# Kernel optimization log

Measured on AMD Instinct MI355X. Metric: run time of the kernel, lower is better.

Reference implementation:

```python
import jax, jax.numpy as jnp
import numpy as np
from jax import lax

B, S, C = 128, 512, 16
V, CV = 50000, 100
E, CE = 100, 30
H = 128        # hidden per direction (hidden_dim=256 // 2)
T = 17         # tagset size
NF = 25        # filters per char-conv
LSTM_IN = E + 3 * NF  # 175


def setup_inputs() -> dict:
    key = jax.random.key(0)
    ks = jax.random.split(key, 25)
    sc = 0.1
    inp = {
        "x": jax.random.randint(ks[0], (B, S), 0, V),
        "char_x": jax.random.randint(ks[1], (B, S, C), 0, CV),
        "tags": jax.random.randint(ks[2], (B, S), 0, T),
        "mask": jnp.ones((B, S), dtype=bool),
        "word_emb": jax.random.normal(ks[3], (V, E), jnp.float32) * sc,
        "char_emb": jax.random.normal(ks[4], (CV, CE), jnp.float32) * sc,
        "conv2_W": jax.random.normal(ks[5], (NF, CE, 2), jnp.float32) * sc,
        "conv2_b": jnp.zeros((NF,), jnp.float32),
        "conv3_W": jax.random.normal(ks[6], (NF, CE, 3), jnp.float32) * sc,
        "conv3_b": jnp.zeros((NF,), jnp.float32),
        "conv4_W": jax.random.normal(ks[7], (NF, CE, 4), jnp.float32) * sc,
        "conv4_b": jnp.zeros((NF,), jnp.float32),
        "W_ih_f": jax.random.normal(ks[8], (4 * H, LSTM_IN), jnp.float32) * sc,
        "W_hh_f": jax.random.normal(ks[9], (4 * H, H), jnp.float32) * sc,
        "b_f": jnp.zeros((4 * H,), jnp.float32),
        "W_ih_b": jax.random.normal(ks[10], (4 * H, LSTM_IN), jnp.float32) * sc,
        "W_hh_b": jax.random.normal(ks[11], (4 * H, H), jnp.float32) * sc,
        "b_b": jnp.zeros((4 * H,), jnp.float32),
        "h2t_W": jax.random.normal(ks[12], (T, 2 * H), jnp.float32) * sc,
        "h2t_b": jnp.zeros((T,), jnp.float32),
        "crf_start": jax.random.normal(ks[13], (T,), jnp.float32) * sc,
        "crf_end": jax.random.normal(ks[14], (T,), jnp.float32) * sc,
        "crf_trans": jax.random.normal(ks[15], (T, T), jnp.float32) * sc,
    }
    return inp


def _char_conv(ce, W, b):
    # ce: [BS, CE, C], W: [O, I, K] -> [BS, O] after relu + max-over-time
    out = lax.conv_general_dilated(ce, W, (1,), 'VALID',
                                   dimension_numbers=('NCH', 'OIH', 'NCH'))
    out = jax.nn.relu(out + b[None, :, None])
    return jnp.max(out, axis=-1)


def _lstm_dir(xs, W_ih, W_hh, b, reverse):
    # xs: [B, S, D] -> hs [B, S, H]; PyTorch gate order i,f,g,o
    xs_t = jnp.swapaxes(xs, 0, 1)  # [S, B, D]
    if reverse:
        xs_t = xs_t[::-1]
    pre = jnp.einsum('sbd,gd->sbg', xs_t, W_ih) + b  # hoist input projection
    h0 = jnp.zeros((xs.shape[0], H), xs.dtype)

    def step(carry, p_t):
        h, c = carry
        g = p_t + h @ W_hh.T
        i = jax.nn.sigmoid(g[:, :H])
        f = jax.nn.sigmoid(g[:, H:2 * H])
        gg = jnp.tanh(g[:, 2 * H:3 * H])
        o = jax.nn.sigmoid(g[:, 3 * H:])
        c = f * c + i * gg
        h = o * jnp.tanh(c)
        return (h, c), h

    _, hs = lax.scan(step, (h0, h0), pre)
    if reverse:
        hs = hs[::-1]
    return jnp.swapaxes(hs, 0, 1)


def _crf_nll(emissions, tags, mask, start, end, trans):
    # emissions [B,S,T]; returns sum over batch of -log p(tags | emissions)
    maskf = mask.astype(emissions.dtype)
    # ---- numerator (gold score) ----
    em_sc = jnp.take_along_axis(emissions, tags[..., None], axis=2)[..., 0]  # [B,S]
    tr_sc = trans[tags[:, :-1], tags[:, 1:]]                                  # [B,S-1]
    last_idx = jnp.sum(mask, axis=1).astype(jnp.int32) - 1
    last_tag = tags[jnp.arange(tags.shape[0]), last_idx]
    score = (start[tags[:, 0]] + em_sc[:, 0]
             + jnp.sum(maskf[:, 1:] * (tr_sc + em_sc[:, 1:]), axis=1)
             + end[last_tag])
    # ---- partition via forward-algorithm scan ----
    em_t = jnp.swapaxes(emissions, 0, 1)  # [S,B,T]
    alpha0 = start[None, :] + em_t[0]     # [B,T]

    def step(alpha, inputs):
        e_t, m_t = inputs  # [B,T], [B]
        new = jax.nn.logsumexp(alpha[:, :, None] + trans[None] + e_t[:, None, :], axis=1)
        alpha = jnp.where(m_t[:, None], new, alpha)
        return alpha, None

    alpha, _ = lax.scan(step, alpha0, (em_t[1:], jnp.swapaxes(mask, 0, 1)[1:]))
    logZ = jax.nn.logsumexp(alpha + end[None, :], axis=1)
    return jnp.sum(logZ - score)


def reference(x, char_x, tags, mask, word_emb, char_emb,
              conv2_W, conv2_b, conv3_W, conv3_b, conv4_W, conv4_b,
              W_ih_f, W_hh_f, b_f, W_ih_b, W_hh_b, b_b,
              h2t_W, h2t_b, crf_start, crf_end, crf_trans):
    # word + char features
    we = word_emb[x]                                     # [B,S,E]
    ce = char_emb[char_x].reshape(B * S, C, CE)          # [BS,C,CE]
    ce = jnp.swapaxes(ce, 1, 2)                          # [BS,CE,C]
    cf = jnp.concatenate([_char_conv(ce, conv2_W, conv2_b),
                          _char_conv(ce, conv3_W, conv3_b),
                          _char_conv(ce, conv4_W, conv4_b)], axis=1)
    cf = cf.reshape(B, S, 3 * NF)
    feats = jnp.concatenate([we, cf], axis=2)            # [B,S,175]
    # BiLSTM
    h_fwd = _lstm_dir(feats, W_ih_f, W_hh_f, b_f, reverse=False)
    h_bwd = _lstm_dir(feats, W_ih_b, W_hh_b, b_b, reverse=True)
    h = jnp.concatenate([h_fwd, h_bwd], axis=2)          # [B,S,2H]
    emissions = jnp.einsum('bsh,th->bst', h, h2t_W) + h2t_b
    # CRF NLL (model returns -crf(...), torchcrf reduction='sum')
    return _crf_nll(emissions, tags, mask, crf_start, crf_end, crf_trans)
```

## Files before the change

kernel.cpp:

```cpp
#include <hip/hip_runtime.h>
#include <hip/hip_bf16.h>

#define B_ 128
#define S_ 512
#define C_ 16
#define E_ 100
#define CE_ 30
#define NF_ 25
#define H_ 128
#define T_ 17
#define LSTM_IN_ 175
#define KP_ 192
#define G4_ 512

typedef __hip_bfloat16 bf16;
typedef short bf16x8 __attribute__((ext_vector_type(8)));
typedef float f32x4 __attribute__((ext_vector_type(4)));

__device__ __forceinline__ float bf2f(unsigned short u){
  union { unsigned int i; float f; } v; v.i = ((unsigned int)u) << 16; return v.f;
}
__device__ __forceinline__ float sigm_f(float x){
  float e = __expf(-x);
  return __builtin_amdgcn_rcpf(1.0f + e);
}
__device__ __forceinline__ float tanh_f(float x){
  x = fminf(15.0f, fmaxf(-15.0f, x));
  float e = __expf(-2.0f*x);
  return (1.0f - e) * __builtin_amdgcn_rcpf(1.0f + e);
}
__device__ __forceinline__ short bf16bits(float f){
  bf16 b = __float2bfloat16(f);
  return *(short*)&b;
}

__global__ __launch_bounds__(256) void zero_pad_kernel(bf16* __restrict__ feats){
  int task = blockIdx.x*256 + threadIdx.x;
  int word = task / 17;
  int col = LSTM_IN_ + (task - word*17);
  feats[(size_t)word*KP_ + col] = __float2bfloat16(0.0f);
}

__global__ __launch_bounds__(256) void word_emb_kernel(const int* __restrict__ x,
    const float* __restrict__ wemb, bf16* __restrict__ feats){
  int word = blockIdx.x*2 + (threadIdx.x>>7);
  int e = threadIdx.x & 127;
  if (e < E_) feats[(size_t)word*KP_ + e] = __float2bfloat16(wemb[(size_t)x[word]*E_ + e]);
}

template<int KW>
__global__ __launch_bounds__(256) void char_conv_kernel(const int* __restrict__ char_x,
    const float* __restrict__ cemb, const float* __restrict__ W,
    const float* __restrict__ bias, bf16* __restrict__ feats, int out_off){
  int task = blockIdx.x*256 + threadIdx.x;
  int word = task / NF_;
  int fi = task - word*NF_;
  const int* cx = char_x + word*C_;
  float w[KW*CE_];
  #pragma unroll
  for (int i=0;i<KW*CE_;++i) w[i] = W[fi*CE_*KW + i];
  const int NP = C_ - KW + 1;
  float acc[C_ - KW + 1];
  #pragma unroll
  for (int p=0;p<NP;++p) acc[p] = 0.0f;
  #pragma unroll
  for (int c=0;c<C_;++c){
    int ci = cx[c];
    const float* ce = cemb + ci*CE_;
    #pragma unroll
    for (int e=0;e<CE_;++e){
      float v = ce[e];
      #pragma unroll
      for (int dx=0;dx<KW;++dx){
        int p = c - dx;
        if (p >= 0 && p < NP) acc[p] = fmaf(v, w[e*KW+dx], acc[p]);
      }
    }
  }
  float m = acc[0];
  #pragma unroll
  for (int p=1;p<NP;++p) m = fmaxf(m, acc[p]);
  feats[(size_t)word*KP_ + out_off + fi] = __float2bfloat16(fmaxf(0.0f, m + bias[fi]));
}

__global__ __launch_bounds__(192) void wpack_kernel(const float* __restrict__ Wf,
    const float* __restrict__ Wb, bf16* __restrict__ wpk){
  int g = blockIdx.x;
  int k = threadIdx.x;
  float v = 0.0f;
  if (k < LSTM_IN_) v = (g < 512) ? Wf[g*LSTM_IN_ + k] : Wb[(g-512)*LSTM_IN_ + k];
  wpk[(size_t)g*KP_ + k] = __float2bfloat16(v);
}

__global__ __launch_bounds__(256) void whh_pack_kernel(const float* __restrict__ Wf,
    const float* __restrict__ Wb, bf16* __restrict__ wpk2){
  int idx = blockIdx.x*256 + threadIdx.x;
  int dir = idx >> 16;
  int rem = idx & 65535;
  const float* W = dir ? Wb : Wf;
  wpk2[idx] = __float2bfloat16(W[rem]);
}

__global__ __launch_bounds__(256, 3) void pre_gemm_mfma(const bf16* __restrict__ feats,
    const bf16* __restrict__ wpk, const float* __restrict__ bf_,
    const float* __restrict__ bb_, bf16* __restrict__ pre){
  __shared__ __align__(16) short lds[16384];
  int br = blockIdx.x;
  int bc = blockIdx.y;
  int dir = bc >> 2;
  int g0 = (bc & 3) * 128;
  const float* bias = dir ? bb_ : bf_;
  int tid = threadIdx.x;
  int wave = tid >> 6, lane = tid & 63;
  int wr = wave >> 1, wc = wave & 1;
  int lrow = lane & 15, lkb = lane >> 4;
  const bf16* Arow = feats + (size_t)br*128*KP_;
  const bf16* Brow = wpk + (size_t)(dir*512 + g0)*KP_;

  auto stage = [&](int bufbase, int k0){
    int s0 = wave*2, s1 = s0 + 1;
    __builtin_amdgcn_global_load_lds(
        (const __attribute__((address_space(1))) void*)(Arow + (size_t)(s0*16 + lrow)*KP_ + k0 + lkb*8),
        (__attribute__((address_space(3))) void*)&lds[bufbase + s0*512], 16, 0, 0);
    __builtin_amdgcn_global_load_lds(
        (const __attribute__((address_space(1))) void*)(Arow + (size_t)(s1*16 + lrow)*KP_ + k0 + lkb*8),
        (__attribute__((address_space(3))) void*)&lds[bufbase + s1*512], 16, 0, 0);
    __builtin_amdgcn_global_load_lds(
        (const __attribute__((address_space(1))) void*)(Brow + (size_t)(s0*16 + lrow)*KP_ + k0 + lkb*8),
        (__attribute__((address_space(3))) void*)&lds[bufbase + 4096 + s0*512], 16, 0, 0);
    __builtin_amdgcn_global_load_lds(
        (const __attribute__((address_space(1))) void*)(Brow + (size_t)(s1*16 + lrow)*KP_ + k0 + lkb*8),
        (__attribute__((address_space(3))) void*)&lds[bufbase + 4096 + s1*512], 16, 0, 0);
  };

  f32x4 acc[4][4];
  #pragma unroll
  for (int i=0;i<4;++i)
    #pragma unroll
    for (int j=0;j<4;++j) acc[i][j] = (f32x4){0.f,0.f,0.f,0.f};

  stage(0, 0);
  __syncthreads();
  int cur = 0;
  for (int t = 0; t < 6; ++t){
    if (t < 5) stage((cur^1)*8192, (t+1)*32);
    const short* A  = &lds[cur*8192];
    const short* Bv = &lds[cur*8192 + 4096];
    bf16x8 af[4], bfr[4];
    #pragma unroll
    for (int i=0;i<4;++i) af[i]  = *(const bf16x8*)&A[(wr*4+i)*512 + lane*8];
    #pragma unroll
    for (int j=0;j<4;++j) bfr[j] = *(const bf16x8*)&Bv[(wc*4+j)*512 + lane*8];
    #pragma unroll
    for (int i=0;i<4;++i)
      #pragma unroll
      for (int j=0;j<4;++j)
        acc[i][j] = __builtin_amdgcn_mfma_f32_16x16x32_bf16(af[i], bfr[j], acc[i][j], 0, 0, 0);
    __syncthreads();
    cur ^= 1;
  }

  int col_l = lane & 15;
  int row_l = (lane >> 4) * 4;
  float bias_v[4];
  #pragma unroll
  for (int j=0;j<4;++j) bias_v[j] = bias[g0 + wc*64 + j*16 + col_l];
  #pragma unroll
  for (int i=0;i<4;++i){
    #pragma unroll
    for (int q=0;q<4;++q){
      int r = wr*64 + i*16 + row_l + q;
      #pragma unroll
      for (int j=0;j<4;++j){
        int cbyte = (wc*64 + j*16 + col_l) * 2;
        int addr = r*256 + (cbyte ^ ((r & 7) << 4));
        *(short*)((char*)lds + addr) = bf16bits(acc[i][j][q] + bias_v[j]);
      }
    }
  }
  __syncthreads();
  int r = tid >> 1, half = tid & 1;
  int word = br*128 + r;
  int bidx = word >> 9, sidx = word & 511;
  bf16* dst = pre + ((size_t)(dir*B_ + bidx)*S_ + sidx)*G4_ + g0 + half*64;
  #pragma unroll
  for (int k=0;k<8;++k){
    int boff = (half*128 + k*16) ^ ((r & 7) << 4);
    int4 v = *(const int4*)((const char*)lds + r*256 + boff);
    *(int4*)((char*)dst + k*16) = v;
  }
}

__global__ __launch_bounds__(512) void lstm_mfma_kernel(
    const bf16* __restrict__ pre, const bf16* __restrict__ wpk2,
    bf16* __restrict__ hs){
  int blk = blockIdx.x;
  int dir = blk & 1;
  int bg  = blk >> 1;
  int tid = threadIdx.x;
  int w = tid >> 6, l = tid & 63;
  int lm = l & 15, lk = l >> 4;
  int gcol = 16*w + lm;

  bf16x8 Bf[4][4];
  {
    const bf16* Wd = wpk2 + (size_t)dir*512*128;
    #pragma unroll
    for (int ct=0; ct<4; ++ct)
      #pragma unroll
      for (int kk=0; kk<4; ++kk)
        Bf[ct][kk] = *(const bf16x8*)(Wd + (ct*128 + gcol)*128 + 32*kk + lk*8);
  }

  __shared__ __align__(16) short h_sh[2][2048];
  for (int i = tid; i < 1024; i += 512) ((int*)h_sh[0])[i] = 0;

  float c[4] = {0.f, 0.f, 0.f, 0.f};
  const bf16* preB = pre + (size_t)(dir*B_ + bg*16) * (S_*G4_);
  bf16* hsB = hs + (size_t)(dir*B_ + bg*16) * (S_*H_);

  unsigned short pfA[16], pfB[16];
  auto LOADPF = [&](unsigned short (&pf)[16], int idx){
    #pragma unroll
    for (int q=0;q<4;++q){
      #pragma unroll
      for (int ct=0;ct<4;++ct)
        pf[q*4+ct] = *(const unsigned short*)(preB
            + ((size_t)((lk*4+q)*S_ + idx))*G4_ + ct*128 + gcol);
    }
  };

  auto STEP = [&](unsigned short (&pfuse)[16], int s, const short* src, short* dst){
    int idx = dir ? (S_-1-s) : s;
    f32x4 a0, a1, a2, a3;
    #pragma unroll
    for (int q=0;q<4;++q){
      a0[q] = bf2f(pfuse[q*4+0]);
      a1[q] = bf2f(pfuse[q*4+1]);
      a2[q] = bf2f(pfuse[q*4+2]);
      a3[q] = bf2f(pfuse[q*4+3]);
    }
    int sp = (s+2 < S_) ? s+2 : s;
    int idxp = dir ? (S_-1-sp) : sp;
    LOADPF(pfuse, idxp);
    #pragma unroll
    for (int kk=0;kk<4;++kk){
      int sc = ((4*kk + lk) ^ lm) & 15;
      bf16x8 af = *(const bf16x8*)((const char*)src + lm*256 + sc*16);
      a0 = __builtin_amdgcn_mfma_f32_16x16x32_bf16(af, Bf[0][kk], a0, 0, 0, 0);
      a1 = __builtin_amdgcn_mfma_f32_16x16x32_bf16(af, Bf[1][kk], a1, 0, 0, 0);
      a2 = __builtin_amdgcn_mfma_f32_16x16x32_bf16(af, Bf[2][kk], a2, 0, 0, 0);
      a3 = __builtin_amdgcn_mfma_f32_16x16x32_bf16(af, Bf[3][kk], a3, 0, 0, 0);
    }
    float hv[4];
    #pragma unroll
    for (int q=0;q<4;++q){
      float iv = sigm_f(a0[q]);
      float fv = sigm_f(a1[q]);
      float gv = tanh_f(a2[q]);
      float ov = sigm_f(a3[q]);
      c[q] = fmaf(fv, c[q], iv*gv);
      hv[q] = ov * tanh_f(c[q]);
    }
    #pragma unroll
    for (int q=0;q<4;++q){
      int b = lk*4 + q;
      int scw = ((gcol >> 3) ^ b) & 15;
      *(short*)((char*)dst + b*256 + scw*16 + (gcol & 7)*2) = bf16bits(hv[q]);
      hsB[((size_t)b*S_ + idx)*H_ + gcol] = __float2bfloat16(hv[q]);
    }
    asm volatile("s_waitcnt lgkmcnt(0)" ::: "memory");
    __builtin_amdgcn_s_barrier();
    asm volatile("" ::: "memory");
  };

  __syncthreads();
  LOADPF(pfA, dir ? (S_-1) : 0);
  LOADPF(pfB, dir ? (S_-2) : 1);
  for (int s = 0; s < S_; s += 2){
    STEP(pfA, s,   h_sh[0], h_sh[1]);
    STEP(pfB, s+1, h_sh[1], h_sh[0]);
  }
}

__global__ __launch_bounds__(256) void emis_kernel(const bf16* __restrict__ hs,
    const float* __restrict__ W, const float* __restrict__ bias, float* __restrict__ em){
  int task = blockIdx.x*256 + threadIdx.x;
  int word = task / T_;
  int t = task - word*T_;
  const ushort4* hf = (const ushort4*)(hs + (size_t)word*H_);
  const ushort4* hb = (const ushort4*)(hs + (size_t)(B_*S_ + word)*H_);
  const float* w0 = W + t*2*H_;
  float acc = bias[t];
  #pragma unroll
  for (int j4=0;j4<32;++j4){
    ushort4 u = hf[j4];
    float4 w4 = *(const float4*)&w0[j4*4];
    acc = fmaf(bf2f(u.x),w4.x,acc); acc = fmaf(bf2f(u.y),w4.y,acc);
    acc = fmaf(bf2f(u.z),w4.z,acc); acc = fmaf(bf2f(u.w),w4.w,acc);
  }
  #pragma unroll
  for (int j4=0;j4<32;++j4){
    ushort4 u = hb[j4];
    float4 w4 = *(const float4*)&w0[H_ + j4*4];
    acc = fmaf(bf2f(u.x),w4.x,acc); acc = fmaf(bf2f(u.y),w4.y,acc);
    acc = fmaf(bf2f(u.z),w4.z,acc); acc = fmaf(bf2f(u.w),w4.w,acc);
  }
  em[(size_t)word*T_ + t] = acc;
}

__global__ __launch_bounds__(256) void score_kernel(const int* __restrict__ tags,
    const float* __restrict__ em, const float* __restrict__ start,
    const float* __restrict__ end_, const float* __restrict__ trans,
    float* __restrict__ score){
  int b = blockIdx.x;
  int tid = threadIdx.x;
  const int* tg = tags + b*S_;
  const float* eb = em + (size_t)b*S_*T_;
  float s = 0.0f;
  for (int t = tid; t < S_; t += 256){
    int cur = tg[t];
    s += eb[(size_t)t*T_ + cur];
    if (t > 0) s += trans[tg[t-1]*T_ + cur];
  }
  if (tid == 0) s += start[tg[0]] + end_[tg[S_-1]];
  __shared__ float red[256];
  red[tid] = s; __syncthreads();
  for (int off=128; off; off>>=1){
    if (tid < off) red[tid] += red[tid+off];
    __syncthreads();
  }
  if (tid == 0) score[b] = red[0];
}

__global__ __launch_bounds__(64) void crf_alpha_kernel(const float* __restrict__ em,
    const float* __restrict__ start, const float* __restrict__ end_,
    const float* __restrict__ trans, float* __restrict__ logZ){
  int b = blockIdx.x;
  int j = threadIdx.x;
  __shared__ float al[T_];
  const float* eb = em + (size_t)b*S_*T_;
  float tcol[T_];
  if (j < T_){
    #pragma unroll
    for (int i=0;i<T_;++i) tcol[i] = trans[i*T_ + j];
    al[j] = start[j] + eb[j];
  }
  float e_cur = (j < T_) ? eb[T_ + j] : 0.0f;
  for (int s=1;s<S_;++s){
    float e_nxt = (j < T_ && s+1 < S_) ? eb[(size_t)(s+1)*T_ + j] : 0.0f;
    if (j < T_){
      float av[T_];
      float m = -1e30f;
      #pragma unroll
      for (int i=0;i<T_;++i){ av[i] = al[i] + tcol[i]; m = fmaxf(m, av[i]); }
      float sum = 0.0f;
      #pragma unroll
      for (int i=0;i<T_;++i) sum += __expf(av[i]-m);
      float nv = m + __logf(sum) + e_cur;
      al[j] = nv;
    }
    e_cur = e_nxt;
  }
  if (j == 0){
    float m = -1e30f;
    float v[T_];
    #pragma unroll
    for (int i=0;i<T_;++i){ v[i] = al[i] + end_[i]; m = fmaxf(m, v[i]); }
    float sum = 0.0f;
    #pragma unroll
    for (int i=0;i<T_;++i) sum += __expf(v[i]-m);
    logZ[b] = m + __logf(sum);
  }
}

__global__ __launch_bounds__(128) void final_kernel(const float* __restrict__ logZ,
    const float* __restrict__ score, float* __restrict__ out){
  int tid = threadIdx.x;
  float v = logZ[tid] - score[tid];
  __shared__ float red[128];
  red[tid] = v; __syncthreads();
  for (int off=64; off; off>>=1){
    if (tid < off) red[tid] += red[tid+off];
    __syncthreads();
  }
  if (tid == 0) out[0] = red[0];
}

extern "C" void kernel_launch(void* const* d_in, const int* in_sizes, int n_in,
                              void* d_out, int out_size, void* d_ws, size_t ws_size,
                              hipStream_t stream) {
  const int*   x       = (const int*)  d_in[0];
  const int*   char_x  = (const int*)  d_in[1];
  const int*   tags    = (const int*)  d_in[2];
  const float* wemb    = (const float*)d_in[4];
  const float* cemb    = (const float*)d_in[5];
  const float* c2W     = (const float*)d_in[6];
  const float* c2b     = (const float*)d_in[7];
  const float* c3W     = (const float*)d_in[8];
  const float* c3b     = (const float*)d_in[9];
  const float* c4W     = (const float*)d_in[10];
  const float* c4b     = (const float*)d_in[11];
  const float* Wih_f   = (const float*)d_in[12];
  const float* Whh_f   = (const float*)d_in[13];
  const float* b_f     = (const float*)d_in[14];
  const float* Wih_b   = (const float*)d_in[15];
  const float* Whh_b   = (const float*)d_in[16];
  const float* b_b     = (const float*)d_in[17];
  const float* h2tW    = (const float*)d_in[18];
  const float* h2tb    = (const float*)d_in[19];
  const float* crf_s   = (const float*)d_in[20];
  const float* crf_e   = (const float*)d_in[21];
  const float* crf_t   = (const float*)d_in[22];
  float* out = (float*)d_out;

  const size_t NEEDED = 168035328ULL;
  if (ws_size < NEEDED) return;
  char* wsb = (char*)d_ws;
  bf16*  pre   = (bf16*)(wsb);
  bf16*  feats = (bf16*)(wsb + 134217728);
  bf16*  wpk   = (bf16*)(wsb + 159383552);
  bf16*  hs    = (bf16*)(wsb + 134217728);
  float* em    = (float*)(wsb);
  float* score = (float*)(wsb + 167772160);
  float* logZ  = (float*)(wsb + 167772672);
  bf16*  wpk2  = (bf16*)(wsb + 167773184);

  zero_pad_kernel<<<4352, 256, 0, stream>>>(feats);
  word_emb_kernel<<<32768, 256, 0, stream>>>(x, wemb, feats);
  char_conv_kernel<2><<<6400, 256, 0, stream>>>(char_x, cemb, c2W, c2b, feats, E_);
  char_conv_kernel<3><<<6400, 256, 0, stream>>>(char_x, cemb, c3W, c3b, feats, E_ + NF_);
  char_conv_kernel<4><<<6400, 256, 0, stream>>>(char_x, cemb, c4W, c4b, feats, E_ + 2*NF_);
  wpack_kernel<<<1024, 192, 0, stream>>>(Wih_f, Wih_b, wpk);
  whh_pack_kernel<<<512, 256, 0, stream>>>(Whh_f, Whh_b, wpk2);
  pre_gemm_mfma<<<dim3(512, 8), 256, 0, stream>>>(feats, wpk, b_f, b_b, pre);
  lstm_mfma_kernel<<<16, 512, 0, stream>>>(pre, wpk2, hs);
  emis_kernel<<<4352, 256, 0, stream>>>(hs, h2tW, h2tb, em);
  score_kernel<<<128, 256, 0, stream>>>(tags, em, crf_s, crf_e, crf_t, score);
  crf_alpha_kernel<<<128, 64, 0, stream>>>(em, crf_s, crf_e, crf_t, logZ);
  final_kernel<<<1, 128, 0, stream>>>(logZ, score, out);
}
```

Before: 1.597 ms.

## Fuse emission projection into LSTM recurrence and pair CRF batches per block

Each LSTM step now computes its direction's share of the hidden-to-tag projection with extra MFMAs on the h tile already held in LDS. Forward and backward partial emissions go to separate buffers and are summed in the score and CRF kernels. This removes the hs write-back and the separate emission kernel. It also strength-reduces the prefetch addressing, packs two batches per CRF block with tree reductions, and adds a few MFMAs to the serial critical path of the recurrence.

```diff
diff --git a/kernel.cpp b/kernel.cpp
--- a/kernel.cpp
+++ b/kernel.cpp
@@ -99,6 +99,16 @@
   int rem = idx & 65535;
   const float* W = dir ? Wb : Wf;
   wpk2[idx] = __float2bfloat16(W[rem]);
+}
+
+__global__ __launch_bounds__(256) void wem_pack_kernel(const float* __restrict__ h2tW,
+    bf16* __restrict__ wem){
+  int idx = blockIdx.x*256 + threadIdx.x;
+  int d = idx >> 12;
+  int rem = idx & 4095;
+  int t = rem >> 7, k = rem & 127;
+  float v = (t < T_) ? h2tW[t*(2*H_) + d*H_ + k] : 0.0f;
+  wem[idx] = __float2bfloat16(v);
 }
 
 __global__ __launch_bounds__(256, 3) void pre_gemm_mfma(const bf16* __restrict__ feats,
@@ -193,7 +203,8 @@
 
 __global__ __launch_bounds__(512) void lstm_mfma_kernel(
     const bf16* __restrict__ pre, const bf16* __restrict__ wpk2,
-    bf16* __restrict__ hs){
+    const bf16* __restrict__ wem, const float* __restrict__ h2tb,
+    float* __restrict__ em_f, float* __restrict__ em_b){
   int blk = blockIdx.x;
   int dir = blk & 1;
   int bg  = blk >> 1;
@@ -208,30 +219,61 @@
     #pragma unroll
     for (int ct=0; ct<4; ++ct)
       #pragma unroll
-      for (int kk=0; kk<4; ++kk)
+      for (int kk=0; kk<4; ++kk){
         Bf[ct][kk] = *(const bf16x8*)(Wd + (ct*128 + gcol)*128 + 32*kk + lk*8);
-  }
+        asm volatile("" : "+v"(Bf[ct][kk]));
+      }
+  }
+  int tag = w*16 + lm;
+  bf16x8 Ef[4];
+  {
+    int trow = (w < 2) ? tag : 0;
+    #pragma unroll
+    for (int kk=0; kk<4; ++kk){
+      Ef[kk] = *(const bf16x8*)(wem + ((size_t)dir*32 + trow)*128 + 32*kk + lk*8);
+      asm volatile("" : "+v"(Ef[kk]));
+    }
+  }
+  float embias = 0.0f;
+  if (dir == 0 && w < 2 && tag < T_) embias = h2tb[tag];
 
   __shared__ __align__(16) short h_sh[2][2048];
   for (int i = tid; i < 1024; i += 512) ((int*)h_sh[0])[i] = 0;
 
   float c[4] = {0.f, 0.f, 0.f, 0.f};
   const bf16* preB = pre + (size_t)(dir*B_ + bg*16) * (S_*G4_);
-  bf16* hsB = hs + (size_t)(dir*B_ + bg*16) * (S_*H_);
+  int sd  = dir ? -1 : 1;
+  int sdG = sd * G4_;
+  int sdT = sd * T_;
+  int idx0 = dir ? (S_-1) : 0;
+
+  const bf16 *p0 = preB + ((size_t)(lk*4+0)*S_ + idx0)*G4_ + gcol;
+  const bf16 *p1 = preB + ((size_t)(lk*4+1)*S_ + idx0)*G4_ + gcol;
+  const bf16 *p2 = preB + ((size_t)(lk*4+2)*S_ + idx0)*G4_ + gcol;
+  const bf16 *p3 = preB + ((size_t)(lk*4+3)*S_ + idx0)*G4_ + gcol;
+
+  float* emBase = (dir ? em_b : em_f) + (size_t)(bg*16)*S_*T_;
+  float *e0 = emBase + ((size_t)(lk*4+0)*S_ + idx0)*T_ + tag;
+  float *e1 = emBase + ((size_t)(lk*4+1)*S_ + idx0)*T_ + tag;
+  float *e2 = emBase + ((size_t)(lk*4+2)*S_ + idx0)*T_ + tag;
+  float *e3 = emBase + ((size_t)(lk*4+3)*S_ + idx0)*T_ + tag;
 
   unsigned short pfA[16], pfB[16];
-  auto LOADPF = [&](unsigned short (&pf)[16], int idx){
-    #pragma unroll
-    for (int q=0;q<4;++q){
-      #pragma unroll
-      for (int ct=0;ct<4;++ct)
-        pf[q*4+ct] = *(const unsigned short*)(preB
-            + ((size_t)((lk*4+q)*S_ + idx))*G4_ + ct*128 + gcol);
-    }
+  auto LOADPF = [&](unsigned short (&pf)[16], bool g){
+    if (g){
+      pf[0]  = *(const unsigned short*)(p0);     pf[1]  = *(const unsigned short*)(p0+128);
+      pf[2]  = *(const unsigned short*)(p0+256); pf[3]  = *(const unsigned short*)(p0+384);
+      pf[4]  = *(const unsigned short*)(p1);     pf[5]  = *(const unsigned short*)(p1+128);
+      pf[6]  = *(const unsigned short*)(p1+256); pf[7]  = *(const unsigned short*)(p1+384);
+      pf[8]  = *(const unsigned short*)(p2);     pf[9]  = *(const unsigned short*)(p2+128);
+      pf[10] = *(const unsigned short*)(p2+256); pf[11] = *(const unsigned short*)(p2+384);
+      pf[12] = *(const unsigned short*)(p3);     pf[13] = *(const unsigned short*)(p3+128);
+      pf[14] = *(const unsigned short*)(p3+256); pf[15] = *(const unsigned short*)(p3+384);
+    }
+    p0 += sdG; p1 += sdG; p2 += sdG; p3 += sdG;
   };
 
   auto STEP = [&](unsigned short (&pfuse)[16], int s, const short* src, short* dst){
-    int idx = dir ? (S_-1-s) : s;
     f32x4 a0, a1, a2, a3;
     #pragma unroll
     for (int q=0;q<4;++q){
@@ -240,18 +282,26 @@
       a2[q] = bf2f(pfuse[q*4+2]);
       a3[q] = bf2f(pfuse[q*4+3]);
     }
-    int sp = (s+2 < S_) ? s+2 : s;
-    int idxp = dir ? (S_-1-sp) : sp;
-    LOADPF(pfuse, idxp);
+    LOADPF(pfuse, s+2 < S_);
+    bf16x8 af[4];
     #pragma unroll
     for (int kk=0;kk<4;++kk){
       int sc = ((4*kk + lk) ^ lm) & 15;
-      bf16x8 af = *(const bf16x8*)((const char*)src + lm*256 + sc*16);
-      a0 = __builtin_amdgcn_mfma_f32_16x16x32_bf16(af, Bf[0][kk], a0, 0, 0, 0);
-      a1 = __builtin_amdgcn_mfma_f32_16x16x32_bf16(af, Bf[1][kk], a1, 0, 0, 0);
-      a2 = __builtin_amdgcn_mfma_f32_16x16x32_bf16(af, Bf[2][kk], a2, 0, 0, 0);
-      a3 = __builtin_amdgcn_mfma_f32_16x16x32_bf16(af, Bf[3][kk], a3, 0, 0, 0);
-    }
+      af[kk] = *(const bf16x8*)((const char*)src + lm*256 + sc*16);
+      a0 = __builtin_amdgcn_mfma_f32_16x16x32_bf16(af[kk], Bf[0][kk], a0, 0, 0, 0);
+      a1 = __builtin_amdgcn_mfma_f32_16x16x32_bf16(af[kk], Bf[1][kk], a1, 0, 0, 0);
+      a2 = __builtin_amdgcn_mfma_f32_16x16x32_bf16(af[kk], Bf[2][kk], a2, 0, 0, 0);
+      a3 = __builtin_amdgcn_mfma_f32_16x16x32_bf16(af[kk], Bf[3][kk], a3, 0, 0, 0);
+    }
+    if (w < 2 && s > 0){
+      f32x4 emq;
+      emq[0]=embias; emq[1]=embias; emq[2]=embias; emq[3]=embias;
+      #pragma unroll
+      for (int kk=0;kk<4;++kk)
+        emq = __builtin_amdgcn_mfma_f32_16x16x32_bf16(af[kk], Ef[kk], emq, 0, 0, 0);
+      if (tag < T_){ *e0 = emq[0]; *e1 = emq[1]; *e2 = emq[2]; *e3 = emq[3]; }
+    }
+    if (s > 0){ e0 += sdT; e1 += sdT; e2 += sdT; e3 += sdT; }
     float hv[4];
     #pragma unroll
     for (int q=0;q<4;++q){
@@ -267,7 +317,6 @@
       int b = lk*4 + q;
       int scw = ((gcol >> 3) ^ b) & 15;
       *(short*)((char*)dst + b*256 + scw*16 + (gcol & 7)*2) = bf16bits(hv[q]);
-      hsB[((size_t)b*S_ + idx)*H_ + gcol] = __float2bfloat16(hv[q]);
     }
     asm volatile("s_waitcnt lgkmcnt(0)" ::: "memory");
     __builtin_amdgcn_s_barrier();
@@ -275,52 +324,39 @@
   };
 
   __syncthreads();
-  LOADPF(pfA, dir ? (S_-1) : 0);
-  LOADPF(pfB, dir ? (S_-2) : 1);
+  LOADPF(pfA, true);
+  LOADPF(pfB, true);
   for (int s = 0; s < S_; s += 2){
     STEP(pfA, s,   h_sh[0], h_sh[1]);
     STEP(pfB, s+1, h_sh[1], h_sh[0]);
   }
-}
-
-__global__ __launch_bounds__(256) void emis_kernel(const bf16* __restrict__ hs,
-    const float* __restrict__ W, const float* __restrict__ bias, float* __restrict__ em){
-  int task = blockIdx.x*256 + threadIdx.x;
-  int word = task / T_;
-  int t = task - word*T_;
-  const ushort4* hf = (const ushort4*)(hs + (size_t)word*H_);
-  const ushort4* hb = (const ushort4*)(hs + (size_t)(B_*S_ + word)*H_);
-  const float* w0 = W + t*2*H_;
-  float acc = bias[t];
-  #pragma unroll
-  for (int j4=0;j4<32;++j4){
-    ushort4 u = hf[j4];
-    float4 w4 = *(const float4*)&w0[j4*4];
-    acc = fmaf(bf2f(u.x),w4.x,acc); acc = fmaf(bf2f(u.y),w4.y,acc);
-    acc = fmaf(bf2f(u.z),w4.z,acc); acc = fmaf(bf2f(u.w),w4.w,acc);
-  }
-  #pragma unroll
-  for (int j4=0;j4<32;++j4){
-    ushort4 u = hb[j4];
-    float4 w4 = *(const float4*)&w0[H_ + j4*4];
-    acc = fmaf(bf2f(u.x),w4.x,acc); acc = fmaf(bf2f(u.y),w4.y,acc);
-    acc = fmaf(bf2f(u.z),w4.z,acc); acc = fmaf(bf2f(u.w),w4.w,acc);
-  }
-  em[(size_t)word*T_ + t] = acc;
+  if (w < 2){
+    f32x4 emq;
+    emq[0]=embias; emq[1]=embias; emq[2]=embias; emq[3]=embias;
+    #pragma unroll
+    for (int kk=0;kk<4;++kk){
+      int sc = ((4*kk + lk) ^ lm) & 15;
+      bf16x8 af = *(const bf16x8*)((const char*)h_sh[0] + lm*256 + sc*16);
+      emq = __builtin_amdgcn_mfma_f32_16x16x32_bf16(af, Ef[kk], emq, 0, 0, 0);
+    }
+    if (tag < T_){ *e0 = emq[0]; *e1 = emq[1]; *e2 = emq[2]; *e3 = emq[3]; }
+  }
 }
 
 __global__ __launch_bounds__(256) void score_kernel(const int* __restrict__ tags,
-    const float* __restrict__ em, const float* __restrict__ start,
+    const float* __restrict__ em_f, const float* __restrict__ em_b,
+    const float* __restrict__ start,
     const float* __restrict__ end_, const float* __restrict__ trans,
     float* __restrict__ score){
   int b = blockIdx.x;
   int tid = threadIdx.x;
   const int* tg = tags + b*S_;
-  const float* eb = em + (size_t)b*S_*T_;
+  const float* ef = em_f + (size_t)b*S_*T_;
+  const float* eb = em_b + (size_t)b*S_*T_;
   float s = 0.0f;
   for (int t = tid; t < S_; t += 256){
     int cur = tg[t];
-    s += eb[(size_t)t*T_ + cur];
+    s += ef[(size_t)t*T_ + cur] + eb[(size_t)t*T_ + cur];
     if (t > 0) s += trans[tg[t-1]*T_ + cur];
   }
   if (tid == 0) s += start[tg[0]] + end_[tg[S_-1]];
@@ -333,40 +369,59 @@
   if (tid == 0) score[b] = red[0];
 }
 
-__global__ __launch_bounds__(64) void crf_alpha_kernel(const float* __restrict__ em,
+__global__ __launch_bounds__(64) void crf_alpha_kernel(const float* __restrict__ em_f,
+    const float* __restrict__ em_b,
     const float* __restrict__ start, const float* __restrict__ end_,
     const float* __restrict__ trans, float* __restrict__ logZ){
-  int b = blockIdx.x;
-  int j = threadIdx.x;
-  __shared__ float al[T_];
-  const float* eb = em + (size_t)b*S_*T_;
+  int pair = blockIdx.x;
+  int lane = threadIdx.x;
+  int half = lane >> 5;
+  int j = lane & 31;
+  int b = pair*2 + half;
+  bool act = j < T_;
+  const float* ef = em_f + (size_t)b*S_*T_;
+  const float* eb = em_b + (size_t)b*S_*T_;
+  __shared__ float al2[2][32];
   float tcol[T_];
-  if (j < T_){
+  if (act){
     #pragma unroll
     for (int i=0;i<T_;++i) tcol[i] = trans[i*T_ + j];
-    al[j] = start[j] + eb[j];
-  }
-  float e_cur = (j < T_) ? eb[T_ + j] : 0.0f;
+    al2[half][j] = start[j] + ef[j] + eb[j];
+  }
+  float ecur = act ? (ef[T_ + j] + eb[T_ + j]) : 0.0f;
+  float enxt = (act && 2 < S_) ? (ef[2*T_ + j] + eb[2*T_ + j]) : 0.0f;
   for (int s=1;s<S_;++s){
-    float e_nxt = (j < T_ && s+1 < S_) ? eb[(size_t)(s+1)*T_ + j] : 0.0f;
-    if (j < T_){
+    float enew = (act && s+2 < S_) ? (ef[(size_t)(s+2)*T_ + j] + eb[(size_t)(s+2)*T_ + j]) : 0.0f;
+    if (act){
       float av[T_];
-      float m = -1e30f;
-      #pragma unroll
-      for (int i=0;i<T_;++i){ av[i] = al[i] + tcol[i]; m = fmaxf(m, av[i]); }
-      float sum = 0.0f;
-      #pragma unroll
-      for (int i=0;i<T_;++i) sum += __expf(av[i]-m);
-      float nv = m + __logf(sum) + e_cur;
-      al[j] = nv;
-    }
-    e_cur = e_nxt;
+      #pragma unroll
+      for (int i=0;i<T_;++i) av[i] = al2[half][i] + tcol[i];
+      float m = fmaxf(
+        fmaxf(fmaxf(fmaxf(av[0],av[1]),fmaxf(av[2],av[3])),
+              fmaxf(fmaxf(av[4],av[5]),fmaxf(av[6],av[7]))),
+        fmaxf(fmaxf(fmaxf(av[8],av[9]),fmaxf(av[10],av[11])),
+              fmaxf(fmaxf(av[12],av[13]),fmaxf(fmaxf(av[14],av[15]),av[16]))));
+      float s0=0.f,s1=0.f,s2=0.f,s3=0.f;
+      #pragma unroll
+      for (int i=0;i<16;i+=4){
+        s0 += __expf(av[i]-m);   s1 += __expf(av[i+1]-m);
+        s2 += __expf(av[i+2]-m); s3 += __expf(av[i+3]-m);
+      }
+      s0 += __expf(av[16]-m);
+      float sum = (s0+s1)+(s2+s3);
+      al2[half][j] = m + __logf(sum) + ecur;
+    }
+    ecur = enxt; enxt = enew;
   }
   if (j == 0){
-    float m = -1e30f;
     float v[T_];
     #pragma unroll
-    for (int i=0;i<T_;++i){ v[i] = al[i] + end_[i]; m = fmaxf(m, v[i]); }
+    for (int i=0;i<T_;++i) v[i] = al2[half][i] + end_[i];
+    float m = fmaxf(
+      fmaxf(fmaxf(fmaxf(v[0],v[1]),fmaxf(v[2],v[3])),
+            fmaxf(fmaxf(v[4],v[5]),fmaxf(v[6],v[7]))),
+      fmaxf(fmaxf(fmaxf(v[8],v[9]),fmaxf(v[10],v[11])),
+            fmaxf(fmaxf(v[12],v[13]),fmaxf(fmaxf(v[14],v[15]),v[16]))));
     float sum = 0.0f;
     #pragma unroll
     for (int i=0;i<T_;++i) sum += __expf(v[i]-m);
@@ -414,17 +469,18 @@
   const float* crf_t   = (const float*)d_in[22];
   float* out = (float*)d_out;
 
-  const size_t NEEDED = 168035328ULL;
+  const size_t NEEDED = 160056320ULL;
   if (ws_size < NEEDED) return;
   char* wsb = (char*)d_ws;
   bf16*  pre   = (bf16*)(wsb);
   bf16*  feats = (bf16*)(wsb + 134217728);
+  float* em_f  = (float*)(wsb + 134217728);
+  float* em_b  = (float*)(wsb + 138674176);
   bf16*  wpk   = (bf16*)(wsb + 159383552);
-  bf16*  hs    = (bf16*)(wsb + 134217728);
-  float* em    = (float*)(wsb);
-  float* score = (float*)(wsb + 167772160);
-  float* logZ  = (float*)(wsb + 167772672);
-  bf16*  wpk2  = (bf16*)(wsb + 167773184);
+  bf16*  wpk2  = (bf16*)(wsb + 159776768);
+  bf16*  wem   = (bf16*)(wsb + 160038912);
+  float* score = (float*)(wsb + 160055296);
+  float* logZ  = (float*)(wsb + 160055808);
 
   zero_pad_kernel<<<4352, 256, 0, stream>>>(feats);
   word_emb_kernel<<<32768, 256, 0, stream>>>(x, wemb, feats);
@@ -433,10 +489,10 @@
   char_conv_kernel<4><<<6400, 256, 0, stream>>>(char_x, cemb, c4W, c4b, feats, E_ + 2*NF_);
   wpack_kernel<<<1024, 192, 0, stream>>>(Wih_f, Wih_b, wpk);
   whh_pack_kernel<<<512, 256, 0, stream>>>(Whh_f, Whh_b, wpk2);
+  wem_pack_kernel<<<32, 256, 0, stream>>>(h2tW, wem);
   pre_gemm_mfma<<<dim3(512, 8), 256, 0, stream>>>(feats, wpk, b_f, b_b, pre);
-  lstm_mfma_kernel<<<16, 512, 0, stream>>>(pre, wpk2, hs);
-  emis_kernel<<<4352, 256, 0, stream>>>(hs, h2tW, h2tb, em);
-  score_kernel<<<128, 256, 0, stream>>>(tags, em, crf_s, crf_e, crf_t, score);
-  crf_alpha_kernel<<<128, 64, 0, stream>>>(em, crf_s, crf_e, crf_t, logZ);
+  lstm_mfma_kernel<<<16, 512, 0, stream>>>(pre, wpk2, wem, h2tb, em_f, em_b);
+  score_kernel<<<128, 256, 0, stream>>>(tags, em_f, em_b, crf_s, crf_e, crf_t, score);
+  crf_alpha_kernel<<<64, 64, 0, stream>>>(em_f, em_b, crf_s, crf_e, crf_t, logZ);
   final_kernel<<<1, 128, 0, stream>>>(logZ, score, out);
 }
```

New measurement: 1.817 ms. 13.8% more time.
